# Optimization experiments

Hardware: AMD Instinct MI355X
Metric: run time of the kernel (lower is better)

The kernel has to match this reference:

```python
import math
import jax, jax.numpy as jnp
import numpy as np
from jax import lax

BIG = 1e20
HUGE = 1e30
SMALL = 1e-10
EPSILON = 0.1
NITER = 50
B, I, J = 256, 256, 256


def setup_inputs() -> dict:
    key = jax.random.key(0)
    # normalized word-pair distances in [0, 1)
    D = jax.random.uniform(key, (B, I, J), dtype=jnp.float32)
    return {"D": D}


def _kl_div(x, y):
    div = x / (y + SMALL)
    return y * (div * jnp.log(div + SMALL) - div + 1.0)


def _wfr_forward(D, epsilon, niter):
    pi2 = jnp.float32(math.pi / 2)
    C = -2.0 * jnp.log(jnp.cos(jnp.minimum(D * 2.0, pi2)) + 1e-5)  # [B,I,J]
    b_, i_, j_ = C.shape
    dx = 1.0 / i_  # uniform weights 1/I
    dy = 1.0 / j_  # uniform weights 1/J
    p_coef = 1.0 / (1.0 + epsilon)

    def K_calc(u, v):
        # K = clamp(exp((-C + u_i + v_j)/eps))
        return jnp.clip(jnp.exp((-C + u[:, :, None] + v[:, None, :]) / epsilon), 0.0, HUGE)

    b0 = jnp.ones((b_, j_), C.dtype)
    u0 = jnp.zeros((b_, i_), C.dtype)
    v0 = jnp.zeros((b_, j_), C.dtype)
    K0 = K_calc(u0, v0)

    def body(ii, carry):
        b, u, v, K = carry
        # row update: s_i = sum_j K_ij * b_j * dy ; mu = 1
        s = jnp.sum(K * (b * dy)[:, None, :], axis=-1)  # [B,I]
        a = jnp.clip((1.0 / (jnp.exp(u) * s)) ** p_coef, 0.0, HUGE)
        # col update: s_j = sum_i K_ij * a_i * dx ; nu = 1
        s2 = jnp.sum(K * (a * dx)[:, :, None], axis=-2)  # [B,J]
        b_new = jnp.clip((1.0 / (jnp.exp(v) * s2)) ** p_coef, 0.0, HUGE)

        rescale = (jnp.max(a) > BIG) | (jnp.max(b_new) > BIG) | (ii == niter - 1)

        def do_rescale(_):
            u2 = epsilon * jnp.log(a) + u
            v2 = epsilon * jnp.log(b_new) + v
            return jnp.ones_like(b_new), u2, v2, K_calc(u2, v2)

        def no_rescale(_):
            return b_new, u, v, K

        return lax.cond(rescale, do_rescale, no_rescale, None)

    b, u, v, K = lax.fori_loop(0, niter, body, (b0, u0, v0, K0))

    # marginal constraint penalties (KL against uniform mu=nu=1)
    row_marg = jnp.sum(K * dy, axis=-1)            # [B,I]
    cons1 = jnp.sum(_kl_div(row_marg, 1.0) * dx, axis=-1)
    col_marg = jnp.sum(K * dx, axis=-2)            # [B,J]
    cons2 = jnp.sum(_kl_div(col_marg, 1.0) * dy, axis=-1)
    transport = jnp.sum(K * C, axis=(-2, -1)) * dx * dy
    p_opt = cons1 + cons2 + transport               # [B]
    return p_opt, K


def reference(D):
    p_opt, _K = _wfr_forward(D, EPSILON, NITER)
    return p_opt
```

## Files before the change

### kernel.cpp

```cpp
#include <hip/hip_runtime.h>
#include <hip/hip_fp16.h>
#include <math.h>

#define NITERS 50

typedef _Float16 h2_t __attribute__((ext_vector_type(2)));

#if defined(__has_builtin)
#if __has_builtin(__builtin_amdgcn_fdot2)
#define HAVE_FDOT2 1
#endif
#endif

__device__ __forceinline__ float fdot2f(unsigned int ka, unsigned int kb, float acc) {
#ifdef HAVE_FDOT2
    return __builtin_amdgcn_fdot2(__builtin_bit_cast(h2_t, ka),
                                  __builtin_bit_cast(h2_t, kb), acc, false);
#else
    h2_t a = __builtin_bit_cast(h2_t, ka);
    h2_t b = __builtin_bit_cast(h2_t, kb);
    return acc + (float)a.x * (float)b.x + (float)a.y * (float)b.y;
#endif
}

__global__ __launch_bounds__(512, 2) void wfr_kernel(const float* __restrict__ D,
                                                     float* __restrict__ out) {
    __shared__ __align__(16) __half Ksh[256 * 256];
    __shared__ __align__(16) float  sh_bf[256];
    __shared__ __align__(16) __half sh_bh[256];
    __shared__ __align__(16) __half sh_ah[256];
    __shared__ __align__(16) float  part[8];

    const int tid = threadIdx.x;
    const int bb  = blockIdx.x;
    char* Kbytes  = reinterpret_cast<char*>(Ksh);

    {
        const float4* D4 = reinterpret_cast<const float4*>(D + (size_t)bb * 65536);
        for (int k = 0; k < 32; ++k) {
            int idx4 = tid + (k << 9);
            float4 d = D4[idx4];
            int i = idx4 >> 6;
            int j = (idx4 & 63) << 2;
            float v0[4] = {d.x, d.y, d.z, d.w};
            float k0[4];
            #pragma unroll
            for (int q = 0; q < 4; ++q) {
                float c = cosf(fminf(v0[q] * 2.0f, 1.57079632679489662f)) + 1e-5f;
                k0[q] = expf(20.0f * logf(c));
            }
            h2_t h01 = { (_Float16)k0[0], (_Float16)k0[1] };
            h2_t h23 = { (_Float16)k0[2], (_Float16)k0[3] };
            uint2 wv;
            wv.x = __builtin_bit_cast(unsigned int, h01);
            wv.y = __builtin_bit_cast(unsigned int, h23);
            int off = (i << 9) + (((j << 1) ^ ((i & 31) << 4)));
            *reinterpret_cast<uint2*>(Kbytes + off) = wv;
        }
    }
    if (tid < 256) {
        sh_bf[tid] = 1.0f;
        sh_bh[tid] = __float2half(1.0f);
    }
    __syncthreads();

    const bool is_row = (tid < 256);
    const int  r  = tid & 255;

    uint4 kreg[32];
    if (is_row) {
        const char* Krow = Kbytes + (r << 9);
        const int rsw = r & 31;
        #pragma unroll
        for (int c = 0; c < 32; ++c)
            kreg[c] = *reinterpret_cast<const uint4*>(Krow + ((c ^ rsw) << 4));
    } else {
        #pragma unroll
        for (int c = 0; c < 32; ++c) {
            unsigned int w[4];
            #pragma unroll
            for (int h = 0; h < 4; ++h) {
                int i0 = (c << 3) + (h << 1);
                int i1 = i0 + 1;
                unsigned int lo = *reinterpret_cast<const unsigned short*>(
                    Kbytes + (i0 << 9) + ((r << 1) ^ ((i0 & 31) << 4)));
                unsigned int hi = *reinterpret_cast<const unsigned short*>(
                    Kbytes + (i1 << 9) + ((r << 1) ^ ((i1 & 31) << 4)));
                w[h] = lo | (hi << 16);
            }
            kreg[c].x = w[0]; kreg[c].y = w[1]; kreg[c].z = w[2]; kreg[c].w = w[3];
        }
    }

    float a_local = 0.0f, b_local = 0.0f, s2m_local = 0.0f;

    for (int it = 0; it < NITERS; ++it) {
        if (is_row) {
            float s0 = 0.0f, s1 = 0.0f, sa = 0.0f, sb = 0.0f;
            #pragma unroll
            for (int c = 0; c < 32; ++c) {
                uint4 bv = *reinterpret_cast<const uint4*>(
                    reinterpret_cast<const char*>(sh_bh) + (c << 4));
                s0 = fdot2f(kreg[c].x, bv.x, s0);
                s1 = fdot2f(kreg[c].y, bv.y, s1);
                sa = fdot2f(kreg[c].z, bv.z, sa);
                sb = fdot2f(kreg[c].w, bv.w, sb);
            }
            float sf = ((s0 + s1) + (sa + sb)) * (1.0f / 256.0f);
            float a  = __powf(sf, -(1.0f / 1.1f));
            a = fminf(a, 1e30f);
            a_local = a;
            sh_ah[r] = __float2half(a);
        }
        __syncthreads();
        if (!is_row) {
            float s0 = 0.0f, s1 = 0.0f, sa = 0.0f, sb = 0.0f;
            #pragma unroll
            for (int c = 0; c < 32; ++c) {
                uint4 av = *reinterpret_cast<const uint4*>(
                    reinterpret_cast<const char*>(sh_ah) + (c << 4));
                s0 = fdot2f(kreg[c].x, av.x, s0);
                s1 = fdot2f(kreg[c].y, av.y, s1);
                sa = fdot2f(kreg[c].z, av.z, sa);
                sb = fdot2f(kreg[c].w, av.w, sb);
            }
            s2m_local = ((s0 + s1) + (sa + sb)) * (1.0f / 256.0f);
            float bn = __powf(s2m_local, -(1.0f / 1.1f));
            bn = fminf(bn, 1e30f);
            b_local = bn;
            sh_bf[r] = bn;
            sh_bh[r] = __float2half(bn);
        }
        __syncthreads();
    }

    float val;
    if (is_row) {
        float s = 0.0f, tp = 0.0f;
        #pragma unroll
        for (int c = 0; c < 32; ++c) {
            float4 blo = *reinterpret_cast<const float4*>(sh_bf + (c << 3));
            float4 bhi = *reinterpret_cast<const float4*>(sh_bf + (c << 3) + 4);
            h2_t p0 = __builtin_bit_cast(h2_t, kreg[c].x);
            h2_t p1 = __builtin_bit_cast(h2_t, kreg[c].y);
            h2_t p2 = __builtin_bit_cast(h2_t, kreg[c].z);
            h2_t p3 = __builtin_bit_cast(h2_t, kreg[c].w);
            float kf[8] = {(float)p0.x,(float)p0.y,(float)p1.x,(float)p1.y,
                           (float)p2.x,(float)p2.y,(float)p3.x,(float)p3.y};
            float bf[8] = {blo.x,blo.y,blo.z,blo.w,bhi.x,bhi.y,bhi.z,bhi.w};
            #pragma unroll
            for (int q = 0; q < 8; ++q) {
                float prod = kf[q] * bf[q];
                s += prod;
                float cl = (kf[q] > 0.0f) ? (-0.1f * __logf(kf[q])) : 0.0f;
                tp = fmaf(prod, cl, tp);
            }
        }
        float row_marg = a_local * s * (1.0f / 256.0f);
        float d1  = row_marg / (1.0f + 1e-10f);
        float kl1 = d1 * __logf(d1 + 1e-10f) - d1 + 1.0f;
        val = kl1 * (1.0f / 256.0f) + (a_local * tp) * (1.0f / 65536.0f);
    } else {
        float col_marg = b_local * s2m_local;
        float d2  = col_marg / (1.0f + 1e-10f);
        float kl2 = d2 * __logf(d2 + 1e-10f) - d2 + 1.0f;
        val = kl2 * (1.0f / 256.0f);
    }

    #pragma unroll
    for (int off = 32; off > 0; off >>= 1)
        val += __shfl_down(val, off, 64);
    if ((tid & 63) == 0) part[tid >> 6] = val;
    __syncthreads();
    if (tid == 0) {
        float t = 0.0f;
        #pragma unroll
        for (int w = 0; w < 8; ++w) t += part[w];
        out[bb] = t;
    }
}

extern "C" void kernel_launch(void* const* d_in, const int* in_sizes, int n_in,
                              void* d_out, int out_size, void* d_ws, size_t ws_size,
                              hipStream_t stream) {
    (void)in_sizes; (void)n_in; (void)d_ws; (void)ws_size; (void)out_size;
    const float* D = reinterpret_cast<const float*>(d_in[0]);
    float* out     = reinterpret_cast<float*>(d_out);
    wfr_kernel<<<dim3(256), dim3(512), 0, stream>>>(D, out);
}
```

Baseline: 216.7 us.

## Replace per-thread fdot2 matvecs with MFMA 16x16x32 across all waves

Rewrites both Sinkhorn matrix-vector products to use MFMA f16 instructions. Every wave now holds K row and column fragments in registers, instead of splitting threads into separate row and column halves. All 512 threads take part in both phases, so the half of the block that previously sat idle in each phase now does work. The cost is redundant MFMA compute, since only one column of each 16-wide B operand matters. There are also extra shared buffers for a, b and s2, and the epilogue reduces through shuffles with a 0.25 factor to correct for lanes being counted four times.

```diff
diff --git a/kernel.cpp b/kernel.cpp
--- a/kernel.cpp
+++ b/kernel.cpp
@@ -4,29 +4,15 @@
 
 #define NITERS 50
 
-typedef _Float16 h2_t __attribute__((ext_vector_type(2)));
-
-#if defined(__has_builtin)
-#if __has_builtin(__builtin_amdgcn_fdot2)
-#define HAVE_FDOT2 1
-#endif
-#endif
-
-__device__ __forceinline__ float fdot2f(unsigned int ka, unsigned int kb, float acc) {
-#ifdef HAVE_FDOT2
-    return __builtin_amdgcn_fdot2(__builtin_bit_cast(h2_t, ka),
-                                  __builtin_bit_cast(h2_t, kb), acc, false);
-#else
-    h2_t a = __builtin_bit_cast(h2_t, ka);
-    h2_t b = __builtin_bit_cast(h2_t, kb);
-    return acc + (float)a.x * (float)b.x + (float)a.y * (float)b.y;
-#endif
-}
+typedef _Float16 half8 __attribute__((ext_vector_type(8)));
+typedef float    f32x4 __attribute__((ext_vector_type(4)));
 
 __global__ __launch_bounds__(512, 2) void wfr_kernel(const float* __restrict__ D,
                                                      float* __restrict__ out) {
     __shared__ __align__(16) __half Ksh[256 * 256];
     __shared__ __align__(16) float  sh_bf[256];
+    __shared__ __align__(16) float  sh_af[256];
+    __shared__ __align__(16) float  sh_s2[256];
     __shared__ __align__(16) __half sh_bh[256];
     __shared__ __align__(16) __half sh_ah[256];
     __shared__ __align__(16) float  part[8];
@@ -49,11 +35,11 @@
                 float c = cosf(fminf(v0[q] * 2.0f, 1.57079632679489662f)) + 1e-5f;
                 k0[q] = expf(20.0f * logf(c));
             }
-            h2_t h01 = { (_Float16)k0[0], (_Float16)k0[1] };
-            h2_t h23 = { (_Float16)k0[2], (_Float16)k0[3] };
+            __half2 h01 = { __float2half(k0[0]), __float2half(k0[1]) };
+            __half2 h23 = { __float2half(k0[2]), __float2half(k0[3]) };
             uint2 wv;
-            wv.x = __builtin_bit_cast(unsigned int, h01);
-            wv.y = __builtin_bit_cast(unsigned int, h23);
+            wv.x = *reinterpret_cast<unsigned int*>(&h01);
+            wv.y = *reinterpret_cast<unsigned int*>(&h23);
             int off = (i << 9) + (((j << 1) ^ ((i & 31) << 4)));
             *reinterpret_cast<uint2*>(Kbytes + off) = wv;
         }
@@ -64,107 +50,137 @@
     }
     __syncthreads();
 
-    const bool is_row = (tid < 256);
-    const int  r  = tid & 255;
-
-    uint4 kreg[32];
-    if (is_row) {
-        const char* Krow = Kbytes + (r << 9);
-        const int rsw = r & 31;
-        #pragma unroll
-        for (int c = 0; c < 32; ++c)
-            kreg[c] = *reinterpret_cast<const uint4*>(Krow + ((c ^ rsw) << 4));
-    } else {
-        #pragma unroll
-        for (int c = 0; c < 32; ++c) {
-            unsigned int w[4];
-            #pragma unroll
-            for (int h = 0; h < 4; ++h) {
-                int i0 = (c << 3) + (h << 1);
-                int i1 = i0 + 1;
-                unsigned int lo = *reinterpret_cast<const unsigned short*>(
-                    Kbytes + (i0 << 9) + ((r << 1) ^ ((i0 & 31) << 4)));
-                unsigned int hi = *reinterpret_cast<const unsigned short*>(
-                    Kbytes + (i1 << 9) + ((r << 1) ^ ((i1 & 31) << 4)));
-                w[h] = lo | (hi << 16);
-            }
-            kreg[c].x = w[0]; kreg[c].y = w[1]; kreg[c].z = w[2]; kreg[c].w = w[3];
-        }
-    }
-
-    float a_local = 0.0f, b_local = 0.0f, s2m_local = 0.0f;
+    const int lane = tid & 63;
+    const int wv   = tid >> 6;
+    const int lr   = lane & 15;
+    const int lg   = lane >> 4;
+    const int rowbase = wv << 5;
+
+    half8 afr[2][8];
+    #pragma unroll
+    for (int blk = 0; blk < 2; ++blk) {
+        int R = rowbase + (blk << 4) + lr;
+        const char* Krow = Kbytes + (R << 9);
+        int swz = (R & 31) << 4;
+        #pragma unroll
+        for (int ch = 0; ch < 8; ++ch)
+            afr[blk][ch] = *reinterpret_cast<const half8*>(
+                Krow + (((ch << 6) + (lg << 4)) ^ swz));
+    }
+    half8 afc[2][8];
+    #pragma unroll
+    for (int blk = 0; blk < 2; ++blk) {
+        int C = rowbase + (blk << 4) + lr;
+        #pragma unroll
+        for (int ch = 0; ch < 8; ++ch) {
+            half8 v;
+            #pragma unroll
+            for (int j = 0; j < 8; ++j) {
+                int i = (ch << 5) + (lg << 3) + j;
+                unsigned short u = *reinterpret_cast<const unsigned short*>(
+                    Kbytes + (i << 9) + (((C << 1) ^ ((i & 31) << 4))));
+                v[j] = __builtin_bit_cast(_Float16, u);
+            }
+            afc[blk][ch] = v;
+        }
+    }
 
     for (int it = 0; it < NITERS; ++it) {
-        if (is_row) {
-            float s0 = 0.0f, s1 = 0.0f, sa = 0.0f, sb = 0.0f;
-            #pragma unroll
-            for (int c = 0; c < 32; ++c) {
-                uint4 bv = *reinterpret_cast<const uint4*>(
-                    reinterpret_cast<const char*>(sh_bh) + (c << 4));
-                s0 = fdot2f(kreg[c].x, bv.x, s0);
-                s1 = fdot2f(kreg[c].y, bv.y, s1);
-                sa = fdot2f(kreg[c].z, bv.z, sa);
-                sb = fdot2f(kreg[c].w, bv.w, sb);
-            }
-            float sf = ((s0 + s1) + (sa + sb)) * (1.0f / 256.0f);
-            float a  = __powf(sf, -(1.0f / 1.1f));
-            a = fminf(a, 1e30f);
-            a_local = a;
-            sh_ah[r] = __float2half(a);
+        {
+            half8 bfr[8];
+            #pragma unroll
+            for (int ch = 0; ch < 8; ++ch)
+                bfr[ch] = *reinterpret_cast<const half8*>(
+                    reinterpret_cast<const char*>(sh_bh) + (ch << 6) + (lg << 4));
+            f32x4 acc0 = {0.f,0.f,0.f,0.f}, acc1 = {0.f,0.f,0.f,0.f};
+            #pragma unroll
+            for (int ch = 0; ch < 8; ++ch) {
+                acc0 = __builtin_amdgcn_mfma_f32_16x16x32_f16(afr[0][ch], bfr[ch], acc0, 0, 0, 0);
+                acc1 = __builtin_amdgcn_mfma_f32_16x16x32_f16(afr[1][ch], bfr[ch], acc1, 0, 0, 0);
+            }
+            if (lr == 0) {
+                #pragma unroll
+                for (int q = 0; q < 4; ++q) {
+                    int   R0 = rowbase + (lg << 2) + q;
+                    float s0 = acc0[q] * (1.0f / 256.0f);
+                    float a0 = fminf(__powf(s0, -(1.0f / 1.1f)), 1e30f);
+                    sh_ah[R0] = __float2half(a0);
+                    sh_af[R0] = a0;
+                    int   R1 = R0 + 16;
+                    float s1 = acc1[q] * (1.0f / 256.0f);
+                    float a1 = fminf(__powf(s1, -(1.0f / 1.1f)), 1e30f);
+                    sh_ah[R1] = __float2half(a1);
+                    sh_af[R1] = a1;
+                }
+            }
         }
         __syncthreads();
-        if (!is_row) {
-            float s0 = 0.0f, s1 = 0.0f, sa = 0.0f, sb = 0.0f;
-            #pragma unroll
-            for (int c = 0; c < 32; ++c) {
-                uint4 av = *reinterpret_cast<const uint4*>(
-                    reinterpret_cast<const char*>(sh_ah) + (c << 4));
-                s0 = fdot2f(kreg[c].x, av.x, s0);
-                s1 = fdot2f(kreg[c].y, av.y, s1);
-                sa = fdot2f(kreg[c].z, av.z, sa);
-                sb = fdot2f(kreg[c].w, av.w, sb);
-            }
-            s2m_local = ((s0 + s1) + (sa + sb)) * (1.0f / 256.0f);
-            float bn = __powf(s2m_local, -(1.0f / 1.1f));
-            bn = fminf(bn, 1e30f);
-            b_local = bn;
-            sh_bf[r] = bn;
-            sh_bh[r] = __float2half(bn);
+        {
+            half8 afrg[8];
+            #pragma unroll
+            for (int ch = 0; ch < 8; ++ch)
+                afrg[ch] = *reinterpret_cast<const half8*>(
+                    reinterpret_cast<const char*>(sh_ah) + (ch << 6) + (lg << 4));
+            f32x4 acc0 = {0.f,0.f,0.f,0.f}, acc1 = {0.f,0.f,0.f,0.f};
+            #pragma unroll
+            for (int ch = 0; ch < 8; ++ch) {
+                acc0 = __builtin_amdgcn_mfma_f32_16x16x32_f16(afc[0][ch], afrg[ch], acc0, 0, 0, 0);
+                acc1 = __builtin_amdgcn_mfma_f32_16x16x32_f16(afc[1][ch], afrg[ch], acc1, 0, 0, 0);
+            }
+            if (lr == 0) {
+                #pragma unroll
+                for (int q = 0; q < 4; ++q) {
+                    int   C0 = rowbase + (lg << 2) + q;
+                    float s20 = acc0[q] * (1.0f / 256.0f);
+                    float b0  = fminf(__powf(s20, -(1.0f / 1.1f)), 1e30f);
+                    sh_bh[C0] = __float2half(b0);
+                    sh_bf[C0] = b0;
+                    sh_s2[C0] = s20;
+                    int   C1 = C0 + 16;
+                    float s21 = acc1[q] * (1.0f / 256.0f);
+                    float b1  = fminf(__powf(s21, -(1.0f / 1.1f)), 1e30f);
+                    sh_bh[C1] = __float2half(b1);
+                    sh_bf[C1] = b1;
+                    sh_s2[C1] = s21;
+                }
+            }
         }
         __syncthreads();
     }
 
-    float val;
-    if (is_row) {
+    float val = 0.0f;
+    #pragma unroll
+    for (int blk = 0; blk < 2; ++blk) {
         float s = 0.0f, tp = 0.0f;
         #pragma unroll
-        for (int c = 0; c < 32; ++c) {
-            float4 blo = *reinterpret_cast<const float4*>(sh_bf + (c << 3));
-            float4 bhi = *reinterpret_cast<const float4*>(sh_bf + (c << 3) + 4);
-            h2_t p0 = __builtin_bit_cast(h2_t, kreg[c].x);
-            h2_t p1 = __builtin_bit_cast(h2_t, kreg[c].y);
-            h2_t p2 = __builtin_bit_cast(h2_t, kreg[c].z);
-            h2_t p3 = __builtin_bit_cast(h2_t, kreg[c].w);
-            float kf[8] = {(float)p0.x,(float)p0.y,(float)p1.x,(float)p1.y,
-                           (float)p2.x,(float)p2.y,(float)p3.x,(float)p3.y};
-            float bf[8] = {blo.x,blo.y,blo.z,blo.w,bhi.x,bhi.y,bhi.z,bhi.w};
-            #pragma unroll
-            for (int q = 0; q < 8; ++q) {
-                float prod = kf[q] * bf[q];
+        for (int ch = 0; ch < 8; ++ch) {
+            const float* bp = sh_bf + (ch << 5) + (lg << 3);
+            float4 b0 = *reinterpret_cast<const float4*>(bp);
+            float4 b1 = *reinterpret_cast<const float4*>(bp + 4);
+            float bf[8] = {b0.x, b0.y, b0.z, b0.w, b1.x, b1.y, b1.z, b1.w};
+            #pragma unroll
+            for (int j = 0; j < 8; ++j) {
+                float kf   = (float)afr[blk][ch][j];
+                float prod = kf * bf[j];
                 s += prod;
-                float cl = (kf[q] > 0.0f) ? (-0.1f * __logf(kf[q])) : 0.0f;
+                float cl = (kf > 0.0f) ? (-0.1f * __logf(kf)) : 0.0f;
                 tp = fmaf(prod, cl, tp);
             }
         }
-        float row_marg = a_local * s * (1.0f / 256.0f);
+        s  += __shfl_xor(s, 16, 64);  s  += __shfl_xor(s, 32, 64);
+        tp += __shfl_xor(tp, 16, 64); tp += __shfl_xor(tp, 32, 64);
+        int   R = rowbase + (blk << 4) + lr;
+        float a = sh_af[R];
+        float row_marg = a * s * (1.0f / 256.0f);
         float d1  = row_marg / (1.0f + 1e-10f);
         float kl1 = d1 * __logf(d1 + 1e-10f) - d1 + 1.0f;
-        val = kl1 * (1.0f / 256.0f) + (a_local * tp) * (1.0f / 65536.0f);
-    } else {
-        float col_marg = b_local * s2m_local;
-        float d2  = col_marg / (1.0f + 1e-10f);
+        val += 0.25f * (kl1 * (1.0f / 256.0f) + (a * tp) * (1.0f / 65536.0f));
+    }
+    if (tid < 256) {
+        float cm  = sh_bf[tid] * sh_s2[tid];
+        float d2  = cm / (1.0f + 1e-10f);
         float kl2 = d2 * __logf(d2 + 1e-10f) - d2 + 1.0f;
-        val = kl2 * (1.0f / 256.0f);
+        val += kl2 * (1.0f / 256.0f);
     }
 
     #pragma unroll
```

Result: slower. 584.5 us (+169.7%).
